# Performance work log

Measured on AMD Instinct MI355X. Metric: run time of the kernel, lower is better.

## Reference

```python
import jax, jax.numpy as jnp
import numpy as np

D_MODEL = 1024
NUM_HEADS = 16
D_K = D_MODEL // NUM_HEADS
B, S = 4, 4096


def setup_inputs() -> dict:
    key = jax.random.key(0)
    ks = jax.random.split(key, 12)
    sc = 1.0 / np.sqrt(D_MODEL)
    inp = {
        "query": jax.random.normal(ks[0], (B, S, D_MODEL), dtype=jnp.float32),
        "key": jax.random.normal(ks[1], (B, S, D_MODEL), dtype=jnp.float32),
        "value": jax.random.normal(ks[2], (B, S, D_MODEL), dtype=jnp.float32),
        "w_q": jax.random.normal(ks[3], (D_MODEL, D_MODEL), dtype=jnp.float32) * sc,
        "b_q": jax.random.normal(ks[4], (D_MODEL,), dtype=jnp.float32) * sc,
        "w_k": jax.random.normal(ks[5], (D_MODEL, D_MODEL), dtype=jnp.float32) * sc,
        "b_k": jax.random.normal(ks[6], (D_MODEL,), dtype=jnp.float32) * sc,
        "w_v": jax.random.normal(ks[7], (D_MODEL, D_MODEL), dtype=jnp.float32) * sc,
        "b_v": jax.random.normal(ks[8], (D_MODEL,), dtype=jnp.float32) * sc,
        "w_o": jax.random.normal(ks[9], (D_MODEL, D_MODEL), dtype=jnp.float32) * sc,
        "b_o": jax.random.normal(ks[10], (D_MODEL,), dtype=jnp.float32) * sc,
    }
    return inp


def reference(query, key, value, w_q, b_q, w_k, b_k, w_v, b_v, w_o, b_o):
    b, s, _ = query.shape
    # projections (torch Linear: x @ W.T + b)
    Q = query @ w_q.T + b_q
    K = key @ w_k.T + b_k
    V = value @ w_v.T + b_v
    # elu+1 feature map
    Q = jax.nn.elu(Q) + 1.0
    K = jax.nn.elu(K) + 1.0
    # [b, h, s, d]
    Q = Q.reshape(b, s, NUM_HEADS, D_K).transpose(0, 2, 1, 3)
    K = K.reshape(b, s, NUM_HEADS, D_K).transpose(0, 2, 1, 3)
    V = V.reshape(b, s, NUM_HEADS, D_K).transpose(0, 2, 1, 3)
    # KV outer-sum: [b, h, d, d]
    KV = jnp.einsum("bhsd,bhse->bhde", K, V)
    Z = jnp.einsum("bhsd,bhde->bhse", Q, KV)  # [b, h, s, d]
    Ksum = K.sum(axis=-2)  # [b, h, d]
    D = jnp.einsum("bhsd,bhd->bhs", Q, Ksum)[..., None]  # [b, h, s, 1]
    Z = Z / (D + 1e-6)
    Z = Z.transpose(0, 2, 1, 3).reshape(b, s, D_MODEL)
    return Z @ w_o.T + b_o
```

## Files before the change

### kernel.cpp

```cpp
#include <hip/hip_runtime.h>
#include <stdint.h>

#define DM 1024
#define NH 16
#define DKH 64
#define BB 4
#define SS 4096
#define MM (BB*SS)

typedef __bf16 bf16x8 __attribute__((ext_vector_type(8)));
typedef float f32x4 __attribute__((ext_vector_type(4)));

__device__ __forceinline__ float bf2f(ushort u) {
  union { uint32_t i; float f; } v; v.i = ((uint32_t)u) << 16; return v.f;
}
__device__ __forceinline__ ushort f2bf(float f) {
  union { float f; uint32_t i; } v; v.f = f;
  uint32_t x = v.i;
  uint32_t r = (x + 0x7fffu + ((x >> 16) & 1u)) >> 16;
  return (ushort)r;
}
__device__ __forceinline__ void unpack8(uint4 u, float* o) {
  o[0] = bf2f((ushort)(u.x & 0xffff)); o[1] = bf2f((ushort)(u.x >> 16));
  o[2] = bf2f((ushort)(u.y & 0xffff)); o[3] = bf2f((ushort)(u.y >> 16));
  o[4] = bf2f((ushort)(u.z & 0xffff)); o[5] = bf2f((ushort)(u.z >> 16));
  o[6] = bf2f((ushort)(u.w & 0xffff)); o[7] = bf2f((ushort)(u.w >> 16));
}
__device__ __forceinline__ void unpack4(uint2 u, float* o) {
  o[0] = bf2f((ushort)(u.x & 0xffff)); o[1] = bf2f((ushort)(u.x >> 16));
  o[2] = bf2f((ushort)(u.y & 0xffff)); o[3] = bf2f((ushort)(u.y >> 16));
}

#define GLL16(g, l) __builtin_amdgcn_global_load_lds( \
    (__attribute__((address_space(1))) void*)(g), \
    (__attribute__((address_space(3))) void*)(l), 16, 0, 0)

__global__ void cast_w4(const float* __restrict__ s0, const float* __restrict__ s1,
                        const float* __restrict__ s2, const float* __restrict__ s3,
                        ushort* __restrict__ d0, ushort* __restrict__ d1,
                        ushort* __restrict__ d2, ushort* __restrict__ d3) {
  const int which = blockIdx.x >> 10;
  const int i = ((blockIdx.x & 1023) * 256 + threadIdx.x) * 4;
  const float* src = which == 0 ? s0 : (which == 1 ? s1 : (which == 2 ? s2 : s3));
  ushort* dst = which == 0 ? d0 : (which == 1 ? d1 : (which == 2 ? d2 : d3));
  float4 v = *reinterpret_cast<const float4*>(src + i);
  ushort4 o; o.x = f2bf(v.x); o.y = f2bf(v.y); o.z = f2bf(v.z); o.w = f2bf(v.w);
  *reinterpret_cast<ushort4*>(dst + i) = o;
}

template<int MODE>
__global__ __launch_bounds__(512, 2) void gemm8p(
    const ushort* __restrict__ A, const ushort* __restrict__ Bw,
    const float* __restrict__ bias, void* __restrict__ Cout) {
  constexpr int K = DM, N = DM;
  constexpr int NT = K / 32;
  __shared__ ushort smem[4][2][256 * 32];
  const int t = threadIdx.x;
  const int lane = t & 63;
  const int w = t >> 6;
  const int id = blockIdx.y * gridDim.x + blockIdx.x;
  const int cpx = (gridDim.x * gridDim.y) >> 3;
  const int swz = (id & 7) * cpx + (id >> 3);
  const int bx = swz % gridDim.x;
  const int by = swz / gridDim.x;
  const int m0 = by * 256, n0 = bx * 256;
  const int wm = w >> 2, wn = w & 3;
  const int fr = lane & 15;
  const int slot = lane >> 4;

  const int gsw = ((t & 3) ^ ((t >> 2) & 3)) * 8;
  const size_t baseA = (size_t)(m0 + (t >> 2)) * K + gsw;
  const size_t baseB = (size_t)(n0 + (t >> 2)) * K + gsw;
  const int ldsoff = w * 512;

  f32x4 acc[8][4] = {};

#define STAGE(tile) { \
    const int _b = (tile) & 3; const size_t _k = (size_t)(tile) * 32; \
    GLL16(A + baseA + _k, &smem[_b][0][ldsoff]); \
    GLL16(A + baseA + (size_t)128 * K + _k, &smem[_b][0][4096 + ldsoff]); \
    GLL16(Bw + baseB + _k, &smem[_b][1][ldsoff]); \
    GLL16(Bw + baseB + (size_t)128 * K + _k, &smem[_b][1][4096 + ldsoff]); }

  STAGE(0); STAGE(1); STAGE(2);
  asm volatile("s_waitcnt vmcnt(8)" ::: "memory");
  __builtin_amdgcn_s_barrier();
  __builtin_amdgcn_sched_barrier(0);

  for (int p = 0; p < NT; ++p) {
    const ushort* At = &smem[p & 3][0][0];
    const ushort* Bt = &smem[p & 3][1][0];
    bf16x8 bfr[4], afr[8];
#pragma unroll
    for (int ni = 0; ni < 4; ++ni) {
      const int row = wn * 64 + ni * 16 + fr;
      bfr[ni] = *reinterpret_cast<const bf16x8*>(Bt + row * 32 + ((slot ^ (fr & 3)) << 3));
    }
#pragma unroll
    for (int mi = 0; mi < 8; ++mi) {
      const int row = wm * 128 + mi * 16 + fr;
      afr[mi] = *reinterpret_cast<const bf16x8*>(At + row * 32 + ((slot ^ (fr & 3)) << 3));
    }
    if (p + 3 < NT) STAGE(p + 3);
    __builtin_amdgcn_s_setprio(1);
#pragma unroll
    for (int mi = 0; mi < 8; ++mi)
#pragma unroll
      for (int ni = 0; ni < 4; ++ni)
        acc[mi][ni] = __builtin_amdgcn_mfma_f32_16x16x32_bf16(afr[mi], bfr[ni], acc[mi][ni], 0, 0, 0);
    __builtin_amdgcn_s_setprio(0);
    if (p < NT - 1) {
      if (p < NT - 3)       asm volatile("s_waitcnt vmcnt(8)" ::: "memory");
      else if (p == NT - 3) asm volatile("s_waitcnt vmcnt(4)" ::: "memory");
      else                  asm volatile("s_waitcnt vmcnt(0)" ::: "memory");
      __builtin_amdgcn_s_barrier();
      __builtin_amdgcn_sched_barrier(0);
    }
  }
#undef STAGE

  const int fq = (lane >> 4) * 4;
  float bv[4];
#pragma unroll
  for (int ni = 0; ni < 4; ++ni) bv[ni] = bias[n0 + wn * 64 + ni * 16 + fr];
#pragma unroll
  for (int mi = 0; mi < 8; ++mi) {
#pragma unroll
    for (int ni = 0; ni < 4; ++ni) {
      const int c = n0 + wn * 64 + ni * 16 + fr;
#pragma unroll
      for (int q = 0; q < 4; ++q) {
        const int r = m0 + wm * 128 + mi * 16 + fq + q;
        float v = acc[mi][ni][q] + bv[ni];
        if constexpr (MODE == 0) v = (v > 0.f) ? (v + 1.f) : __expf(v);
        if constexpr (MODE == 2) {
          reinterpret_cast<float*>(Cout)[(size_t)r * N + c] = v;
        } else {
          reinterpret_cast<ushort*>(Cout)[(size_t)r * N + c] = f2bf(v);
        }
      }
    }
  }
}

__global__ __launch_bounds__(512, 2) void gemm8pa(
    const float* __restrict__ Q32, const float* __restrict__ K32,
    const float* __restrict__ V32,
    const ushort* __restrict__ Wq, const ushort* __restrict__ Wk,
    const ushort* __restrict__ Wv,
    const float* __restrict__ bq, const float* __restrict__ bk,
    const float* __restrict__ bv_,
    ushort* __restrict__ Qp, ushort* __restrict__ Kp, ushort* __restrict__ Vp) {
  constexpr int K = DM, N = DM;
  constexpr int NT = K / 32;
  __shared__ float  smemA[3][256 * 32];
  __shared__ ushort smemB[3][256 * 32];
  const int bz = blockIdx.z;
  const float*  A32  = bz == 0 ? Q32 : (bz == 1 ? K32 : V32);
  const ushort* Bw   = bz == 0 ? Wq  : (bz == 1 ? Wk  : Wv);
  const float*  bias = bz == 0 ? bq  : (bz == 1 ? bk  : bv_);
  ushort*       Cout = bz == 0 ? Qp  : (bz == 1 ? Kp  : Vp);
  const bool do_elu = (bz != 2);

  const int t = threadIdx.x;
  const int lane = t & 63;
  const int w = t >> 6;
  const int id = blockIdx.y * gridDim.x + blockIdx.x;
  const int cpx = (gridDim.x * gridDim.y) >> 3;
  const int swz = (id & 7) * cpx + (id >> 3);
  const int bx = swz % gridDim.x;
  const int by = swz / gridDim.x;
  const int m0 = by * 256, n0 = bx * 256;
  const int wm = w >> 1, wn = w & 1;
  const int fr = lane & 15;
  const int slot = lane >> 4;

  const int gcolA = (((t & 7) ^ ((t >> 3) & 7)) << 2);
  const size_t baseAf = (size_t)(m0 + (t >> 3)) * K + gcolA;
  const int gsw = ((t & 3) ^ ((t >> 2) & 3)) * 8;
  const size_t baseB = (size_t)(n0 + (t >> 2)) * K + gsw;
  const int ldsoffB = w * 512;

  const int rx = lane & 7;
  const int sA0 = (((2 * slot) ^ rx) << 2);
  const int sA1 = (((2 * slot + 1) ^ rx) << 2);
  const int sB = ((slot ^ (fr & 3)) << 3);

  f32x4 acc[4][8] = {};

#define STAGEA(tile) { \
    const int _b = (tile) % 3; const size_t _k = (size_t)(tile) * 32; \
    GLL16(A32 + baseAf + _k,                      &smemA[_b][w * 256]); \
    GLL16(A32 + baseAf + (size_t) 64 * K + _k,    &smemA[_b][2048 + w * 256]); \
    GLL16(A32 + baseAf + (size_t)128 * K + _k,    &smemA[_b][4096 + w * 256]); \
    GLL16(A32 + baseAf + (size_t)192 * K + _k,    &smemA[_b][6144 + w * 256]); }
#define STAGEB(tile) { \
    const int _b = (tile) % 3; const size_t _k = (size_t)(tile) * 32; \
    GLL16(Bw + baseB + _k,                  &smemB[_b][ldsoffB]); \
    GLL16(Bw + baseB + (size_t)128 * K + _k, &smemB[_b][4096 + ldsoffB]); }

  STAGEA(0); STAGEB(0); STAGEA(1); STAGEB(1);
  asm volatile("s_waitcnt vmcnt(6)" ::: "memory");
  __builtin_amdgcn_s_barrier();
  __builtin_amdgcn_sched_barrier(0);

  for (int p = 0; p < NT; ++p) {
    const float*  At = &smemA[p % 3][0];
    const ushort* Bt = &smemB[p % 3][0];
    bf16x8 bfr[8], afr[4];
#pragma unroll
    for (int ni = 0; ni < 8; ++ni) {
      const int row = wn * 128 + ni * 16 + fr;
      bfr[ni] = *reinterpret_cast<const bf16x8*>(Bt + row * 32 + sB);
    }
#pragma unroll
    for (int mi = 0; mi < 4; ++mi) {
      const float* rbase = At + (wm * 64 + mi * 16 + fr) * 32;
      f32x4 a0 = *reinterpret_cast<const f32x4*>(rbase + sA0);
      f32x4 a1 = *reinterpret_cast<const f32x4*>(rbase + sA1);
      uint4 uu;
      asm("v_cvt_pk_bf16_f32 %0, %1, %2" : "=v"(uu.x) : "v"(a0[0]), "v"(a0[1]));
      asm("v_cvt_pk_bf16_f32 %0, %1, %2" : "=v"(uu.y) : "v"(a0[2]), "v"(a0[3]));
      asm("v_cvt_pk_bf16_f32 %0, %1, %2" : "=v"(uu.z) : "v"(a1[0]), "v"(a1[1]));
      asm("v_cvt_pk_bf16_f32 %0, %1, %2" : "=v"(uu.w) : "v"(a1[2]), "v"(a1[3]));
      afr[mi] = *reinterpret_cast<bf16x8*>(&uu);
    }
    if (p + 2 < NT) { STAGEA(p + 2); STAGEB(p + 2); }
    __builtin_amdgcn_s_setprio(1);
#pragma unroll
    for (int mi = 0; mi < 4; ++mi)
#pragma unroll
      for (int ni = 0; ni < 8; ++ni)
        acc[mi][ni] = __builtin_amdgcn_mfma_f32_16x16x32_bf16(afr[mi], bfr[ni], acc[mi][ni], 0, 0, 0);
    __builtin_amdgcn_s_setprio(0);
    if (p < NT - 1) {
      if (p < NT - 2) asm volatile("s_waitcnt vmcnt(6)" ::: "memory");
      else            asm volatile("s_waitcnt vmcnt(0)" ::: "memory");
      __builtin_amdgcn_s_barrier();
      __builtin_amdgcn_sched_barrier(0);
    }
  }
#undef STAGEA
#undef STAGEB

  const int fq = (lane >> 4) * 4;
  float bvv[8];
#pragma unroll
  for (int ni = 0; ni < 8; ++ni) bvv[ni] = bias[n0 + wn * 128 + ni * 16 + fr];
#pragma unroll
  for (int mi = 0; mi < 4; ++mi) {
#pragma unroll
    for (int ni = 0; ni < 8; ++ni) {
      const int c = n0 + wn * 128 + ni * 16 + fr;
#pragma unroll
      for (int q = 0; q < 4; ++q) {
        const int r = m0 + wm * 64 + mi * 16 + fq + q;
        float v = acc[mi][ni][q] + bvv[ni];
        if (do_elu) v = (v > 0.f) ? (v + 1.f) : __expf(v);
        Cout[(size_t)r * N + c] = f2bf(v);
      }
    }
  }
}

__global__ __launch_bounds__(256) void kv_kernel(
    const ushort* __restrict__ Kp, const ushort* __restrict__ Vp,
    float* __restrict__ KVpart, float* __restrict__ Kspart) {
  __shared__ ushort KL[4][64][64];
  __shared__ ushort VL[4][64][64];
  __shared__ float REDK[4][64];
  const int bh = blockIdx.x;
  const int chunk = blockIdx.y;
  const int b = bh >> 4, h = bh & 15;
  const int t = threadIdx.x;
  const int w = t >> 6, lane = t & 63;
  const int d0 = (lane >> 2) * 4;
  const int e0 = (lane & 3) * 16;
  const int srow = lane >> 3;
  const int scol = (lane & 7) * 8;

  float acc[4][16] = {};
  float ks[4] = {};

  ushort* lk = &KL[w][0][0];
  ushort* lv = &VL[w][0][0];
  const int s_wave = chunk * 512 + w * 128;

  for (int tile = 0; tile < 2; ++tile) {
    const int s0 = s_wave + tile * 64;
    const size_t gbase = (size_t)(b * SS + s0 + srow) * DM + h * 64 + scol;
    asm volatile("s_waitcnt lgkmcnt(0)" ::: "memory");
#pragma unroll
    for (int it = 0; it < 8; ++it) {
      GLL16(Kp + gbase + (size_t)it * 8 * DM, lk + it * 512);
      GLL16(Vp + gbase + (size_t)it * 8 * DM, lv + it * 512);
    }
    asm volatile("s_waitcnt vmcnt(0)" ::: "memory");
    __builtin_amdgcn_sched_barrier(0);

#pragma unroll 2
    for (int s = 0; s < 64; ++s) {
      float kf[4], vf[16];
      uint2 uk = *reinterpret_cast<const uint2*>(&KL[w][s][d0]);
      uint4 uv0 = *reinterpret_cast<const uint4*>(&VL[w][s][e0]);
      uint4 uv1 = *reinterpret_cast<const uint4*>(&VL[w][s][e0 + 8]);
      unpack4(uk, kf);
      unpack8(uv0, vf);
      unpack8(uv1, vf + 8);
#pragma unroll
      for (int i = 0; i < 4; ++i) {
        ks[i] += kf[i];
#pragma unroll
        for (int j = 0; j < 16; ++j) acc[i][j] += kf[i] * vf[j];
      }
    }
  }

  float* rl = reinterpret_cast<float*>(&KL[w][0][0]);
  float* rh = reinterpret_cast<float*>(&VL[w][0][0]);
#pragma unroll
  for (int i = 0; i < 4; ++i) {
    const int d = d0 + i;
    float* dst = (d < 32) ? (rl + d * 64 + e0) : (rh + (d - 32) * 64 + e0);
#pragma unroll
    for (int j4 = 0; j4 < 4; ++j4) {
      float4 v = { acc[i][j4*4+0], acc[i][j4*4+1], acc[i][j4*4+2], acc[i][j4*4+3] };
      *reinterpret_cast<float4*>(dst + j4 * 4) = v;
    }
  }
  if ((lane & 3) == 0) {
    float4 v = { ks[0], ks[1], ks[2], ks[3] };
    *reinterpret_cast<float4*>(&REDK[w][d0]) = v;
  }
  __syncthreads();

  float* KLf = reinterpret_cast<float*>(&KL[0][0][0]);
  float* VLf = reinterpret_cast<float*>(&VL[0][0][0]);
  float* out = KVpart + ((size_t)chunk * 64 + bh) * 4096;
  for (int e = t; e < 4096; e += 256) {
    const int d = e >> 6;
    const float* bp = (d < 32) ? KLf : VLf;
    const int off = (d < 32) ? e : (e - 2048);
    out[e] = bp[off] + bp[2048 + off] + bp[4096 + off] + bp[6144 + off];
  }
  if (t < 64) {
    Kspart[((size_t)chunk * 64 + bh) * 64 + t] =
        REDK[0][t] + REDK[1][t] + REDK[2][t] + REDK[3][t];
  }
}

__global__ __launch_bounds__(256) void kvreduce_kernel(
    const float* __restrict__ KVpart, const float* __restrict__ Kspart,
    ushort* __restrict__ KVTx) {
  const int idx = blockIdx.x * 256 + threadIdx.x;
  const int bh = idx >> 12;
  const int d = (idx >> 6) & 63;
  const int e = idx & 63;
  float s = 0.f;
#pragma unroll
  for (int c = 0; c < 8; ++c) s += KVpart[(size_t)c * (64 * 4096) + idx];
  KVTx[(size_t)bh * 5120 + e * 64 + d] = f2bf(s);
  if (idx < 64 * 64) {
    float s2 = 0.f;
#pragma unroll
    for (int c = 0; c < 8; ++c) s2 += Kspart[(size_t)c * 4096 + idx];
    KVTx[(size_t)(idx >> 6) * 5120 + 4096 + (idx & 63)] = f2bf(s2);
  }
  if (idx < 64 * 960) {
    const int bh2 = idx / 960;
    const int rem = idx % 960;
    KVTx[(size_t)bh2 * 5120 + 4160 + rem] = 0;
  }
}

__global__ __launch_bounds__(256) void z_mfma_kernel(
    const ushort* __restrict__ Qp, const ushort* __restrict__ KVTx,
    ushort* __restrict__ Zn) {
  const int bh = blockIdx.y;
  const int b = bh >> 4, h = bh & 15;
  const int t = threadIdx.x;
  const int w = t >> 6, lane = t & 63;
  const int fr = lane & 15;
  const int kq = (lane >> 4) * 8;
  const int s0 = blockIdx.x * 128 + w * 32;

  const ushort* kvb = KVTx + (size_t)bh * 5120;
  bf16x8 bfrag[5][2];
#pragma unroll
  for (int ni = 0; ni < 5; ++ni)
#pragma unroll
    for (int ks = 0; ks < 2; ++ks)
      bfrag[ni][ks] = *reinterpret_cast<const bf16x8*>(kvb + (ni * 16 + fr) * 64 + ks * 32 + kq);

  f32x4 acc[2][5] = {};
  const size_t arow = (size_t)(b * SS + s0 + fr) * DM + h * 64;
#pragma unroll
  for (int mi = 0; mi < 2; ++mi) {
#pragma unroll
    for (int ks = 0; ks < 2; ++ks) {
      bf16x8 a = *reinterpret_cast<const bf16x8*>(Qp + arow + (size_t)mi * 16 * DM + ks * 32 + kq);
#pragma unroll
      for (int ni = 0; ni < 5; ++ni)
        acc[mi][ni] = __builtin_amdgcn_mfma_f32_16x16x32_bf16(a, bfrag[ni][ks], acc[mi][ni], 0, 0, 0);
    }
  }

#pragma unroll
  for (int mi = 0; mi < 2; ++mi) {
#pragma unroll
    for (int q = 0; q < 4; ++q) {
      const float dv = __shfl(acc[mi][4][q], lane & 48);
      const float inv = 1.f / (dv + 1e-6f);
      const int r = s0 + mi * 16 + (lane >> 4) * 4 + q;
      ushort* orow = Zn + (size_t)(b * SS + r) * DM + h * 64;
#pragma unroll
      for (int ni = 0; ni < 4; ++ni)
        orow[ni * 16 + fr] = f2bf(acc[mi][ni][q] * inv);
    }
  }
}

extern "C" void kernel_launch(void* const* d_in, const int* in_sizes, int n_in,
                              void* d_out, int out_size, void* d_ws, size_t ws_size,
                              hipStream_t stream) {
  const float* query = (const float*)d_in[0];
  const float* key_  = (const float*)d_in[1];
  const float* value = (const float*)d_in[2];
  const float* w_q = (const float*)d_in[3];
  const float* b_q = (const float*)d_in[4];
  const float* w_k = (const float*)d_in[5];
  const float* b_k = (const float*)d_in[6];
  const float* w_v = (const float*)d_in[7];
  const float* b_v = (const float*)d_in[8];
  const float* w_o = (const float*)d_in[9];
  const float* b_o = (const float*)d_in[10];

  char* ws = (char*)d_ws;
  const size_t NX = (size_t)MM * DM;
  ushort* Wq = (ushort*)ws; ws += (size_t)DM * DM * 2;
  ushort* Wk = (ushort*)ws; ws += (size_t)DM * DM * 2;
  ushort* Wv = (ushort*)ws; ws += (size_t)DM * DM * 2;
  ushort* Wo = (ushort*)ws; ws += (size_t)DM * DM * 2;
  ushort* Qp = (ushort*)ws; ws += NX * 2;
  ushort* Kp = (ushort*)ws; ws += NX * 2;
  ushort* Vp = (ushort*)ws; ws += NX * 2;
  float*  KVpart = (float*)ws; ws += (size_t)8 * 64 * 4096 * 4;
  float*  Kspart = (float*)ws; ws += (size_t)8 * 4096 * 4;
  ushort* KVTx = (ushort*)ws; ws += (size_t)64 * 80 * 64 * 2;
  ushort* Zn = (ushort*)ws; ws += NX * 2;

  cast_w4<<<4 * 1024, 256, 0, stream>>>(w_q, w_k, w_v, w_o, Wq, Wk, Wv, Wo);

  dim3 gg3(DM / 256, MM / 256, 3);
  gemm8pa<<<gg3, 512, 0, stream>>>(query, key_, value, Wq, Wk, Wv,
                                   b_q, b_k, b_v, Qp, Kp, Vp);

  kv_kernel<<<dim3(64, 8), 256, 0, stream>>>(Kp, Vp, KVpart, Kspart);
  kvreduce_kernel<<<1024, 256, 0, stream>>>(KVpart, Kspart, KVTx);
  z_mfma_kernel<<<dim3(32, 64), 256, 0, stream>>>(Qp, KVTx, Zn);

  dim3 gg(DM / 256, MM / 256);
  gemm8p<2><<<gg, 512, 0, stream>>>(Zn, Wo, b_o, d_out);
}
```

Before: 254.3 us.

## Interleave LDS B-fragment loads, global prefetch and MFMA in four barrier-separated phases

Splits the GEMM main loop into four phases. Each phase loads two B fragments from LDS, issues part of the next tile's global-to-LDS prefetch, hits a workgroup barrier, and then runs 8 MFMAs. The aim is to spread LDS reads and global load issue across the MFMA stream instead of front-loading them, and to cut register pressure from holding all 8 B fragments at once. In exchange it adds three extra s_barrier calls per iteration, which can cost waves time waiting at each barrier.

```diff
diff --git a/kernel.cpp b/kernel.cpp
--- a/kernel.cpp
+++ b/kernel.cpp
@@ -188,18 +188,32 @@
 
   f32x4 acc[4][8] = {};
 
-#define STAGEA(tile) { \
+#define STAGEA01(tile) { \
     const int _b = (tile) % 3; const size_t _k = (size_t)(tile) * 32; \
-    GLL16(A32 + baseAf + _k,                      &smemA[_b][w * 256]); \
-    GLL16(A32 + baseAf + (size_t) 64 * K + _k,    &smemA[_b][2048 + w * 256]); \
-    GLL16(A32 + baseAf + (size_t)128 * K + _k,    &smemA[_b][4096 + w * 256]); \
-    GLL16(A32 + baseAf + (size_t)192 * K + _k,    &smemA[_b][6144 + w * 256]); }
+    GLL16(A32 + baseAf + _k,                   &smemA[_b][w * 256]); \
+    GLL16(A32 + baseAf + (size_t) 64 * K + _k, &smemA[_b][2048 + w * 256]); }
+#define STAGEA23(tile) { \
+    const int _b = (tile) % 3; const size_t _k = (size_t)(tile) * 32; \
+    GLL16(A32 + baseAf + (size_t)128 * K + _k, &smemA[_b][4096 + w * 256]); \
+    GLL16(A32 + baseAf + (size_t)192 * K + _k, &smemA[_b][6144 + w * 256]); }
 #define STAGEB(tile) { \
     const int _b = (tile) % 3; const size_t _k = (size_t)(tile) * 32; \
     GLL16(Bw + baseB + _k,                  &smemB[_b][ldsoffB]); \
     GLL16(Bw + baseB + (size_t)128 * K + _k, &smemB[_b][4096 + ldsoffB]); }
-
-  STAGEA(0); STAGEB(0); STAGEA(1); STAGEB(1);
+#define BPAIR(n0i) \
+    b0 = *reinterpret_cast<const bf16x8*>(Bt + (wn * 128 + (n0i) * 16 + fr) * 32 + sB); \
+    b1 = *reinterpret_cast<const bf16x8*>(Bt + (wn * 128 + (n0i + 1) * 16 + fr) * 32 + sB);
+#define MMAPAIR(n0i) \
+    __builtin_amdgcn_s_setprio(1); \
+    _Pragma("unroll") \
+    for (int mi = 0; mi < 4; ++mi) { \
+      acc[mi][n0i]     = __builtin_amdgcn_mfma_f32_16x16x32_bf16(afr[mi], b0, acc[mi][n0i], 0, 0, 0); \
+      acc[mi][n0i + 1] = __builtin_amdgcn_mfma_f32_16x16x32_bf16(afr[mi], b1, acc[mi][n0i + 1], 0, 0, 0); \
+    } \
+    __builtin_amdgcn_s_setprio(0);
+
+  STAGEA01(0); STAGEA23(0); STAGEB(0);
+  STAGEA01(1); STAGEA23(1); STAGEB(1);
   asm volatile("s_waitcnt vmcnt(6)" ::: "memory");
   __builtin_amdgcn_s_barrier();
   __builtin_amdgcn_sched_barrier(0);
@@ -207,12 +221,8 @@
   for (int p = 0; p < NT; ++p) {
     const float*  At = &smemA[p % 3][0];
     const ushort* Bt = &smemB[p % 3][0];
-    bf16x8 bfr[8], afr[4];
-#pragma unroll
-    for (int ni = 0; ni < 8; ++ni) {
-      const int row = wn * 128 + ni * 16 + fr;
-      bfr[ni] = *reinterpret_cast<const bf16x8*>(Bt + row * 32 + sB);
-    }
+    const bool stg = (p + 2 < NT);
+    bf16x8 afr[4], b0, b1;
 #pragma unroll
     for (int mi = 0; mi < 4; ++mi) {
       const float* rbase = At + (wm * 64 + mi * 16 + fr) * 32;
@@ -225,14 +235,21 @@
       asm("v_cvt_pk_bf16_f32 %0, %1, %2" : "=v"(uu.w) : "v"(a1[2]), "v"(a1[3]));
       afr[mi] = *reinterpret_cast<bf16x8*>(&uu);
     }
-    if (p + 2 < NT) { STAGEA(p + 2); STAGEB(p + 2); }
-    __builtin_amdgcn_s_setprio(1);
-#pragma unroll
-    for (int mi = 0; mi < 4; ++mi)
-#pragma unroll
-      for (int ni = 0; ni < 8; ++ni)
-        acc[mi][ni] = __builtin_amdgcn_mfma_f32_16x16x32_bf16(afr[mi], bfr[ni], acc[mi][ni], 0, 0, 0);
-    __builtin_amdgcn_s_setprio(0);
+    BPAIR(0);
+    if (stg) STAGEA01(p + 2);
+    __builtin_amdgcn_s_barrier();
+    MMAPAIR(0);
+    BPAIR(2);
+    if (stg) STAGEA23(p + 2);
+    __builtin_amdgcn_s_barrier();
+    MMAPAIR(2);
+    BPAIR(4);
+    if (stg) STAGEB(p + 2);
+    __builtin_amdgcn_s_barrier();
+    MMAPAIR(4);
+    BPAIR(6);
+    __builtin_amdgcn_s_barrier();
+    MMAPAIR(6);
     if (p < NT - 1) {
       if (p < NT - 2) asm volatile("s_waitcnt vmcnt(6)" ::: "memory");
       else            asm volatile("s_waitcnt vmcnt(0)" ::: "memory");
@@ -240,8 +257,11 @@
       __builtin_amdgcn_sched_barrier(0);
     }
   }
-#undef STAGEA
+#undef MMAPAIR
+#undef BPAIR
 #undef STAGEB
+#undef STAGEA23
+#undef STAGEA01
 
   const int fq = (lane >> 4) * 4;
   float bvv[8];
```

Measured after the change: 287.8 us. 13.2% more time.
